# Performance work log

Measured on AMD Instinct MI355X. Metric: run time of the kernel, lower is better.

Reference implementation:

```python
import jax, jax.numpy as jnp
import numpy as np

L, N, H = 32768, 256, 256


def _binop(ei, ej):
    a_i, bu_i = ei
    a_j, bu_j = ej
    return (a_j * a_i, a_j * bu_i + bu_j)


def setup_inputs() -> dict:
    key = jax.random.key(0)
    ks = jax.random.split(key, 9)
    # Param values follow init_lru_parameters statistics for numerical sanity.
    u1 = jax.random.uniform(ks[0], (N,), minval=1e-3, maxval=1.0)
    u2 = jax.random.uniform(ks[1], (N,), minval=1e-3, maxval=1.0)
    nu_log = jnp.log(-0.5 * jnp.log(u1))
    theta_log = jnp.log(6.28 * u2)
    B_re = jax.random.normal(ks[2], (N, H)) / np.sqrt(2.0 * H)
    B_im = jax.random.normal(ks[3], (N, H)) / np.sqrt(2.0 * H)
    C_re = jax.random.normal(ks[4], (H, N)) / np.sqrt(1.0 * N)
    C_im = jax.random.normal(ks[5], (H, N)) / np.sqrt(1.0 * N)
    D = jax.random.normal(ks[6], (H,))
    diag_lambda = jnp.exp(-jnp.exp(nu_log) + 1j * jnp.exp(theta_log))
    gamma_log = jnp.log(jnp.sqrt(1.0 - jnp.abs(diag_lambda) ** 2))
    x = jax.random.normal(ks[7], (L, H), dtype=jnp.float32)
    f32 = lambda a: a.astype(jnp.float32)
    return {"x": x, "nu_log": f32(nu_log), "theta_log": f32(theta_log),
            "B_re": f32(B_re), "B_im": f32(B_im), "C_re": f32(C_re),
            "C_im": f32(C_im), "D": f32(D), "gamma_log": f32(gamma_log)}


def reference(x, nu_log, theta_log, B_re, B_im, C_re, C_im, D, gamma_log):
    # Diagonal complex LRU: x_t = Lambda * x_{t-1} + B_norm u_t ; y_t = Re(C x_t) + D*u_t
    Lambda = jnp.exp(-jnp.exp(nu_log) + 1j * jnp.exp(theta_log))        # (N,) complex
    B_norm = (B_re + 1j * B_im) * jnp.exp(gamma_log)[:, None]           # (N,H)
    C = C_re + 1j * C_im                                                # (H,N)
    Bu = x.astype(B_norm.dtype) @ B_norm.T                              # (L,N) complex
    Lam_el = jnp.broadcast_to(Lambda[None, :], Bu.shape)                # (L,N)
    _, states = jax.lax.associative_scan(_binop, (Lam_el, Bu))          # (L,N) complex
    y = (states @ C.T).real + x * D                                     # (L,H) real
    return y
```

## Files before the change

kernel.cpp:

```cpp
#include <hip/hip_runtime.h>

#define L_SEQ 32768
#define NDIM 256
#define HDIM 256
#define NCAT 512
#define LC 64
#define NCHUNK 512

typedef unsigned short u16;
typedef unsigned int u32;
typedef __bf16 bf16x8 __attribute__((ext_vector_type(8)));
typedef float f32x4 __attribute__((ext_vector_type(4)));
typedef __attribute__((address_space(3))) void lds_void;
typedef const __attribute__((address_space(1))) void gbl_void;

__device__ __forceinline__ u16 f2bf(float f) {
  u32 u = __builtin_bit_cast(u32, f);
  u = u + 0x7fffu + ((u >> 16) & 1u);
  return (u16)(u >> 16);
}
__device__ __forceinline__ float bf2f(u16 v) {
  u32 u = ((u32)v) << 16;
  return __builtin_bit_cast(float, u);
}

__global__ __launch_bounds__(256) void prep_kernel(
    const float* __restrict__ x,
    const float* __restrict__ nu_log, const float* __restrict__ theta_log,
    const float* __restrict__ B_re, const float* __restrict__ B_im,
    const float* __restrict__ C_re, const float* __restrict__ C_im,
    const float* __restrict__ gamma_log,
    u16* __restrict__ x_bf, u16* __restrict__ Bcat, u16* __restrict__ Ccat,
    float2* __restrict__ lam, float2* __restrict__ lam64)
{
  const int blk = blockIdx.x, tid = threadIdx.x;
  if (blk < 2048) {
    const float4* src = ((const float4*)x) + (size_t)blk * 1024;
    ushort4* dst = ((ushort4*)x_bf) + (size_t)blk * 1024;
#pragma unroll
    for (int j = 0; j < 4; ++j) {
      float4 v = src[j * 256 + tid];
      dst[j * 256 + tid] = make_ushort4(f2bf(v.x), f2bf(v.y), f2bf(v.z), f2bf(v.w));
    }
  } else if (blk < 2560) {
    int b2 = blk - 2048;
    int jj = b2 >> 1, p = b2 & 1;
    float g = expf(gamma_log[jj]);
    const float* src = (p ? B_im : B_re) + (size_t)jj * HDIM;
    Bcat[(size_t)b2 * HDIM + tid] = f2bf(src[tid] * g);
  } else if (blk < 2816) {
    int h = blk - 2560;
#pragma unroll
    for (int half = 0; half < 2; ++half) {
      int nc = half * 256 + tid;
      int jj = nc >> 1, p = nc & 1;
      float v = p ? -C_im[(size_t)h * NDIM + jj] : C_re[(size_t)h * NDIM + jj];
      Ccat[(size_t)h * NCAT + nc] = f2bf(v);
    }
  } else {
    float nu_e = expf(nu_log[tid]);
    float th = expf(theta_log[tid]);
    float r = expf(-nu_e);
    lam[tid] = make_float2(r * cosf(th), r * sinf(th));
    float r64 = expf(-(float)LC * nu_e);
    float ph = (float)LC * th;
    lam64[tid] = make_float2(r64 * cosf(ph), r64 * sinf(ph));
  }
}

template <bool EPI_XD, bool OUT_BF16>
__global__ __launch_bounds__(256) void gemm_bt_kernel(
    const u16* __restrict__ A,
    const u16* __restrict__ Bm,
    void* __restrict__ Cout,
    int M, int N, int K,
    const u16* __restrict__ xbf, const float* __restrict__ Dv)
{
  constexpr int BM = 128, BN = 128, BK = 32;
  __shared__ u16 lA[BM * BK];
  __shared__ u16 lB[BN * BK];
  const int tid = threadIdx.x;
  const int lane = tid & 63, wave = tid >> 6;
  const int bn = blockIdx.x, bm = blockIdx.y;
  const int row0 = bm * BM, col0 = bn * BN;
  const int wm = (wave >> 1) * 64, wn = (wave & 1) * 64;
  const int fr = lane & 15, fo = (lane >> 4) * 8;

  f32x4 acc[4][4] = {};
  const int nkt = K / BK;
  for (int kt = 0; kt < nkt; ++kt) {
    const int k0 = kt * BK;
#pragma unroll
    for (int j = 0; j < 2; ++j) {
      int chunk = j * 256 + tid;
      int r = chunk >> 2, c = chunk & 3;
      const u16* ga = A + (size_t)(row0 + r) * K + (k0 + c * 8);
      const u16* gb = Bm + (size_t)(col0 + r) * K + (k0 + c * 8);
      __builtin_amdgcn_global_load_lds((gbl_void*)ga, (lds_void*)&lA[chunk * 8], 16, 0, 0);
      __builtin_amdgcn_global_load_lds((gbl_void*)gb, (lds_void*)&lB[chunk * 8], 16, 0, 0);
    }
    __syncthreads();

    bf16x8 af[4], bfr[4];
#pragma unroll
    for (int i = 0; i < 4; ++i) {
      af[i]  = *reinterpret_cast<const bf16x8*>(&lA[(wm + i * 16 + fr) * BK + fo]);
      bfr[i] = *reinterpret_cast<const bf16x8*>(&lB[(wn + i * 16 + fr) * BK + fo]);
    }
#pragma unroll
    for (int i = 0; i < 4; ++i)
#pragma unroll
      for (int j = 0; j < 4; ++j)
        acc[i][j] = __builtin_amdgcn_mfma_f32_16x16x32_bf16(af[i], bfr[j], acc[i][j], 0, 0, 0);
    __syncthreads();
  }

  const int fq = lane >> 4;
#pragma unroll
  for (int i = 0; i < 4; ++i)
#pragma unroll
    for (int j = 0; j < 4; ++j) {
      int cg = col0 + wn + j * 16 + fr;
      float dvc = EPI_XD ? Dv[cg] : 0.f;
#pragma unroll
      for (int r = 0; r < 4; ++r) {
        int rg = row0 + wm + i * 16 + fq * 4 + r;
        float v = acc[i][j][r];
        if (EPI_XD) v += bf2f(xbf[(size_t)rg * N + cg]) * dvc;
        if (OUT_BF16) ((u16*)Cout)[(size_t)rg * N + cg] = f2bf(v);
        else          ((float*)Cout)[(size_t)rg * N + cg] = v;
      }
    }
}

__global__ __launch_bounds__(256) void scan_carry_kernel(
    const ushort2* __restrict__ Bu2, const float2* __restrict__ lam,
    float2* __restrict__ carry)
{
  const int n = threadIdx.x, b = blockIdx.x;
  const float2 la = lam[n];
  float sre = 0.f, sim = 0.f;
  const ushort2* p = Bu2 + (size_t)b * LC * NDIM + n;
#pragma unroll 8
  for (int j = 0; j < LC; ++j) {
    ushort2 bu = p[(size_t)j * NDIM];
    float bre = bf2f(bu.x), bim = bf2f(bu.y);
    float nre = la.x * sre - la.y * sim + bre;
    float nim = la.x * sim + la.y * sre + bim;
    sre = nre; sim = nim;
  }
  carry[(size_t)b * NDIM + n] = make_float2(sre, sim);
}

__global__ __launch_bounds__(512) void carry_scan_kernel(
    const float2* __restrict__ carry, const float2* __restrict__ lam64,
    float2* __restrict__ corr)
{
  __shared__ float4 e[NCHUNK];
  const int n = blockIdx.x;
  const int b = threadIdx.x;
  float2 a = lam64[n];
  float2 v = carry[(size_t)b * NDIM + n];
  e[b] = make_float4(a.x, a.y, v.x, v.y);
  __syncthreads();
#pragma unroll
  for (int d = 1; d < NCHUNK; d <<= 1) {
    float4 prev;
    if (b >= d) prev = e[b - d];
    __syncthreads();
    if (b >= d) {
      float2 ap = make_float2(prev.x, prev.y), vp = make_float2(prev.z, prev.w);
      float2 na, nv;
      na.x = a.x * ap.x - a.y * ap.y;
      na.y = a.x * ap.y + a.y * ap.x;
      nv.x = a.x * vp.x - a.y * vp.y + v.x;
      nv.y = a.x * vp.y + a.y * vp.x + v.y;
      a = na; v = nv;
      e[b] = make_float4(a.x, a.y, v.x, v.y);
    }
    __syncthreads();
  }
  if (b == 0) corr[n] = make_float2(0.f, 0.f);
  if (b < NCHUNK - 1) corr[(size_t)(b + 1) * NDIM + n] = v;
}

__global__ __launch_bounds__(256) void scan_apply_kernel(
    const ushort2* __restrict__ Bu2, const float2* __restrict__ lam,
    const float2* __restrict__ corr, u16* __restrict__ Sbf)
{
  const int n = threadIdx.x, b = blockIdx.x;
  const float2 la = lam[n];
  const float2 c = corr[(size_t)b * NDIM + n];
  float sre = c.x, sim = c.y;
  const ushort2* p = Bu2 + (size_t)b * LC * NDIM + n;
  ushort2* q = ((ushort2*)Sbf) + (size_t)b * LC * NDIM + n;
#pragma unroll 4
  for (int j = 0; j < LC; ++j) {
    ushort2 bu = p[(size_t)j * NDIM];
    float bre = bf2f(bu.x), bim = bf2f(bu.y);
    float nre = la.x * sre - la.y * sim + bre;
    float nim = la.x * sim + la.y * sre + bim;
    sre = nre; sim = nim;
    q[(size_t)j * NDIM] = make_ushort2(f2bf(sre), f2bf(sim));
  }
}

extern "C" void kernel_launch(void* const* d_in, const int* in_sizes, int n_in,
                              void* d_out, int out_size, void* d_ws, size_t ws_size,
                              hipStream_t stream)
{
  (void)in_sizes; (void)n_in; (void)out_size; (void)ws_size;
  const float* x         = (const float*)d_in[0];
  const float* nu_log    = (const float*)d_in[1];
  const float* theta_log = (const float*)d_in[2];
  const float* B_re      = (const float*)d_in[3];
  const float* B_im      = (const float*)d_in[4];
  const float* C_re      = (const float*)d_in[5];
  const float* C_im      = (const float*)d_in[6];
  const float* Dv        = (const float*)d_in[7];
  const float* gamma_log = (const float*)d_in[8];

  char* ws = (char*)d_ws;
  u16*    x_bf  = (u16*)ws;
  u16*    s_bf  = (u16*)(ws + ((size_t)16 << 20));
  u16*    Bu_bf = (u16*)(ws + ((size_t)48 << 20));
  u16*    Bcat  = (u16*)(ws + ((size_t)80 << 20));
  u16*    Ccat  = (u16*)(ws + ((size_t)80 << 20) + 262144);
  float2* lam   = (float2*)(ws + ((size_t)80 << 20) + 524288);
  float2* lam64 = (float2*)(ws + ((size_t)80 << 20) + 524288 + 4096);
  float2* carry = (float2*)(ws + ((size_t)81 << 20));
  float2* corr  = (float2*)(ws + ((size_t)82 << 20));

  prep_kernel<<<2817, 256, 0, stream>>>(x, nu_log, theta_log, B_re, B_im,
                                        C_re, C_im, gamma_log,
                                        x_bf, Bcat, Ccat, lam, lam64);

  gemm_bt_kernel<false, true><<<dim3(NCAT / 128, L_SEQ / 128), 256, 0, stream>>>(
      x_bf, Bcat, Bu_bf, L_SEQ, NCAT, HDIM, nullptr, nullptr);

  scan_carry_kernel<<<NCHUNK, 256, 0, stream>>>((const ushort2*)Bu_bf, lam, carry);
  carry_scan_kernel<<<NDIM, 512, 0, stream>>>(carry, lam64, corr);
  scan_apply_kernel<<<NCHUNK, 256, 0, stream>>>((const ushort2*)Bu_bf, lam, corr, s_bf);

  gemm_bt_kernel<true, false><<<dim3(HDIM / 128, L_SEQ / 128), 256, 0, stream>>>(
      s_bf, Ccat, (float*)d_out, L_SEQ, HDIM, NCAT, x_bf, Dv);
}
```

Measured before the change: 82.77 us.

## Fuse scan-apply into output GEMM, computing states in LDS per tile

Removes the separate scan_apply kernel and the bf16 state buffer. Each output GEMM block (64 rows) loads its Bu chunk into LDS, runs the sequential recurrence from the chunk correction, and writes the states back into LDS with an XOR swizzle. It then uses them directly as the A operand for the MFMA against C. This saves a full global write and read of the state tensor and one launch. The cost is that the scan is recomputed by both column blocks, and the larger 64KB LDS tile may reduce occupancy.

```diff
diff --git a/kernel.cpp b/kernel.cpp
--- a/kernel.cpp
+++ b/kernel.cpp
@@ -68,13 +68,11 @@
   }
 }
 
-template <bool EPI_XD, bool OUT_BF16>
-__global__ __launch_bounds__(256) void gemm_bt_kernel(
+__global__ __launch_bounds__(256) void gemm1_kernel(
     const u16* __restrict__ A,
     const u16* __restrict__ Bm,
-    void* __restrict__ Cout,
-    int M, int N, int K,
-    const u16* __restrict__ xbf, const float* __restrict__ Dv)
+    u16* __restrict__ Cout,
+    int M, int N, int K)
 {
   constexpr int BM = 128, BN = 128, BK = 32;
   __shared__ u16 lA[BM * BK];
@@ -121,14 +119,10 @@
 #pragma unroll
     for (int j = 0; j < 4; ++j) {
       int cg = col0 + wn + j * 16 + fr;
-      float dvc = EPI_XD ? Dv[cg] : 0.f;
 #pragma unroll
       for (int r = 0; r < 4; ++r) {
         int rg = row0 + wm + i * 16 + fq * 4 + r;
-        float v = acc[i][j][r];
-        if (EPI_XD) v += bf2f(xbf[(size_t)rg * N + cg]) * dvc;
-        if (OUT_BF16) ((u16*)Cout)[(size_t)rg * N + cg] = f2bf(v);
-        else          ((float*)Cout)[(size_t)rg * N + cg] = v;
+        Cout[(size_t)rg * N + cg] = f2bf(acc[i][j][r]);
       }
     }
 }
@@ -184,25 +178,109 @@
   if (b < NCHUNK - 1) corr[(size_t)(b + 1) * NDIM + n] = v;
 }
 
-__global__ __launch_bounds__(256) void scan_apply_kernel(
-    const ushort2* __restrict__ Bu2, const float2* __restrict__ lam,
-    const float2* __restrict__ corr, u16* __restrict__ Sbf)
-{
-  const int n = threadIdx.x, b = blockIdx.x;
-  const float2 la = lam[n];
-  const float2 c = corr[(size_t)b * NDIM + n];
-  float sre = c.x, sim = c.y;
-  const ushort2* p = Bu2 + (size_t)b * LC * NDIM + n;
-  ushort2* q = ((ushort2*)Sbf) + (size_t)b * LC * NDIM + n;
-#pragma unroll 4
-  for (int j = 0; j < LC; ++j) {
-    ushort2 bu = p[(size_t)j * NDIM];
-    float bre = bf2f(bu.x), bim = bf2f(bu.y);
-    float nre = la.x * sre - la.y * sim + bre;
-    float nim = la.x * sim + la.y * sre + bim;
-    sre = nre; sim = nim;
-    q[(size_t)j * NDIM] = make_ushort2(f2bf(sre), f2bf(sim));
-  }
+__global__ __launch_bounds__(256) void gemm2_kernel(
+    const u16* __restrict__ Bu,
+    const u16* __restrict__ Cc,
+    const float2* __restrict__ lam,
+    const float2* __restrict__ corr,
+    const u16* __restrict__ xbf,
+    const float* __restrict__ Dv,
+    float* __restrict__ out)
+{
+  constexpr int BM = 64, BN = 128, BK = 32, K = NCAT;
+  __shared__ u16 sT[BM * K];
+  __shared__ u16 lB1[BN * BK];
+  const int tid = threadIdx.x;
+  const int lane = tid & 63, wave = tid >> 6;
+  const int bn = blockIdx.x, bm = blockIdx.y;
+  const int row0 = bm * BM, col0 = bn * BN;
+  const int wm = (wave >> 1) * 32, wn = (wave & 1) * 64;
+  const int fr = lane & 15, fq = lane >> 4;
+  char* sb = (char*)sT;
+
+#pragma unroll
+  for (int j = 0; j < 16; ++j) {
+    int q = j * 256 + tid;
+    int row = q >> 6, off = q & 63;
+    const u16* g = Bu + (size_t)(row0 + row) * NCAT + off * 8;
+    __builtin_amdgcn_global_load_lds((gbl_void*)g, (lds_void*)&sT[q * 8], 16, 0, 0);
+  }
+  float2 la = lam[tid];
+  float2 c0 = corr[(size_t)bm * NDIM + tid];
+  __syncthreads();
+
+  {
+    float sre = c0.x, sim = c0.y;
+    ushort2 buf[8], nbuf[8];
+    const int lb = tid * 4;
+#pragma unroll
+    for (int s = 0; s < 8; ++s) buf[s] = *(const ushort2*)(sb + s * 1024 + lb);
+#pragma unroll
+    for (int b8 = 0; b8 < 8; ++b8) {
+      if (b8 < 7) {
+#pragma unroll
+        for (int s = 0; s < 8; ++s)
+          nbuf[s] = *(const ushort2*)(sb + (b8 * 8 + 8 + s) * 1024 + lb);
+      }
+#pragma unroll
+      for (int s = 0; s < 8; ++s) {
+        int row = b8 * 8 + s;
+        float bre = bf2f(buf[s].x), bim = bf2f(buf[s].y);
+        float nre = la.x * sre - la.y * sim + bre;
+        float nim = la.x * sim + la.y * sre + bim;
+        sre = nre; sim = nim;
+        *(ushort2*)(sb + row * 1024 + (lb ^ ((row & 7) << 4))) =
+            make_ushort2(f2bf(sre), f2bf(sim));
+      }
+#pragma unroll
+      for (int s = 0; s < 8; ++s) buf[s] = nbuf[s];
+    }
+  }
+  __syncthreads();
+
+  f32x4 acc[2][4] = {};
+#pragma unroll 1
+  for (int kt = 0; kt < 16; ++kt) {
+#pragma unroll
+    for (int j = 0; j < 2; ++j) {
+      int q = j * 256 + tid;
+      int row = q >> 2, c = q & 3;
+      const u16* g = Cc + (size_t)(col0 + row) * K + kt * BK + c * 8;
+      __builtin_amdgcn_global_load_lds((gbl_void*)g, (lds_void*)&lB1[q * 8], 16, 0, 0);
+    }
+    __syncthreads();
+
+    bf16x8 af[2], bfr[4];
+#pragma unroll
+    for (int i = 0; i < 2; ++i) {
+      int row = wm + i * 16 + fr;
+      int wb = kt * 64 + fq * 16;
+      af[i] = *(const bf16x8*)(sb + row * 1024 + (wb ^ ((row & 7) << 4)));
+    }
+#pragma unroll
+    for (int j = 0; j < 4; ++j)
+      bfr[j] = *(const bf16x8*)(&lB1[(wn + j * 16 + fr) * BK + fq * 8]);
+#pragma unroll
+    for (int i = 0; i < 2; ++i)
+#pragma unroll
+      for (int j = 0; j < 4; ++j)
+        acc[i][j] = __builtin_amdgcn_mfma_f32_16x16x32_bf16(af[i], bfr[j], acc[i][j], 0, 0, 0);
+    __syncthreads();
+  }
+
+#pragma unroll
+  for (int i = 0; i < 2; ++i)
+#pragma unroll
+    for (int j = 0; j < 4; ++j) {
+      int cg = col0 + wn + j * 16 + fr;
+      float dvc = Dv[cg];
+#pragma unroll
+      for (int r = 0; r < 4; ++r) {
+        int rg = row0 + wm + i * 16 + fq * 4 + r;
+        float v = acc[i][j][r] + bf2f(xbf[(size_t)rg * HDIM + cg]) * dvc;
+        out[(size_t)rg * HDIM + cg] = v;
+      }
+    }
 }
 
 extern "C" void kernel_launch(void* const* d_in, const int* in_sizes, int n_in,
@@ -222,26 +300,25 @@
 
   char* ws = (char*)d_ws;
   u16*    x_bf  = (u16*)ws;
-  u16*    s_bf  = (u16*)(ws + ((size_t)16 << 20));
-  u16*    Bu_bf = (u16*)(ws + ((size_t)48 << 20));
-  u16*    Bcat  = (u16*)(ws + ((size_t)80 << 20));
-  u16*    Ccat  = (u16*)(ws + ((size_t)80 << 20) + 262144);
-  float2* lam   = (float2*)(ws + ((size_t)80 << 20) + 524288);
-  float2* lam64 = (float2*)(ws + ((size_t)80 << 20) + 524288 + 4096);
-  float2* carry = (float2*)(ws + ((size_t)81 << 20));
-  float2* corr  = (float2*)(ws + ((size_t)82 << 20));
+  u16*    Bu_bf = (u16*)(ws + ((size_t)16 << 20));
+  u16*    Bcat  = (u16*)(ws + ((size_t)48 << 20));
+  u16*    Ccat  = (u16*)(ws + ((size_t)48 << 20) + 262144);
+  float2* lam   = (float2*)(ws + ((size_t)48 << 20) + 524288);
+  float2* lam64 = (float2*)(ws + ((size_t)48 << 20) + 524288 + 4096);
+  float2* carry = (float2*)(ws + ((size_t)49 << 20));
+  float2* corr  = (float2*)(ws + ((size_t)50 << 20));
 
   prep_kernel<<<2817, 256, 0, stream>>>(x, nu_log, theta_log, B_re, B_im,
                                         C_re, C_im, gamma_log,
                                         x_bf, Bcat, Ccat, lam, lam64);
 
-  gemm_bt_kernel<false, true><<<dim3(NCAT / 128, L_SEQ / 128), 256, 0, stream>>>(
-      x_bf, Bcat, Bu_bf, L_SEQ, NCAT, HDIM, nullptr, nullptr);
+  gemm1_kernel<<<dim3(NCAT / 128, L_SEQ / 128), 256, 0, stream>>>(
+      x_bf, Bcat, Bu_bf, L_SEQ, NCAT, HDIM);
 
   scan_carry_kernel<<<NCHUNK, 256, 0, stream>>>((const ushort2*)Bu_bf, lam, carry);
+
   carry_scan_kernel<<<NDIM, 512, 0, stream>>>(carry, lam64, corr);
-  scan_apply_kernel<<<NCHUNK, 256, 0, stream>>>((const ushort2*)Bu_bf, lam, corr, s_bf);
-
-  gemm_bt_kernel<true, false><<<dim3(HDIM / 128, L_SEQ / 128), 256, 0, stream>>>(
-      s_bf, Ccat, (float*)d_out, L_SEQ, HDIM, NCAT, x_bf, Dv);
-}
+
+  gemm2_kernel<<<dim3(HDIM / 128, L_SEQ / 64), 256, 0, stream>>>(
+      Bu_bf, Ccat, lam, corr, x_bf, Dv, (float*)d_out);
+}
```

Result: no change. 83.58 us (+1.0%).
